# Kernel tuning notes

Hardware: AMD Instinct MI355X
Metric: run time of the kernel (lower is better)

## Reference

```python
import jax, jax.numpy as jnp
import numpy as np

B, S, E, H, L = 8, 1024, 1024, 16, 2
D = E // H
EPS = 1e-5
THRESH = 0.5


def layer_norm(x, g, b):
    mu = x.mean(-1, keepdims=True)
    var = ((x - mu) ** 2).mean(-1, keepdims=True)
    return (x - mu) * jax.lax.rsqrt(var + EPS) * g + b


def mha(x, w_in, w_out):
    # x: [B,S,E]; w_in: [3E,E]; w_out: [E,E] (no biases, PyTorch MultiheadAttention bias=False)
    qkv = x @ w_in.T  # [B,S,3E]
    q, k, v = jnp.split(qkv, 3, axis=-1)
    q = q.reshape(q.shape[0], q.shape[1], H, D).transpose(0, 2, 1, 3)
    k = k.reshape(k.shape[0], k.shape[1], H, D).transpose(0, 2, 1, 3)
    v = v.reshape(v.shape[0], v.shape[1], H, D).transpose(0, 2, 1, 3)
    scores = jnp.einsum('bhqd,bhkd->bhqk', q, k) / jnp.sqrt(jnp.float32(D)).astype(x.dtype)
    attn = jax.nn.softmax(scores, axis=-1)
    out = jnp.einsum('bhqk,bhkd->bhqd', attn, v)
    out = out.transpose(0, 2, 1, 3).reshape(x.shape[0], x.shape[1], E)
    return out @ w_out.T


def thinking_layer(x, w_in, w_out, ffn1, ffn2, g1, b1, g2, b2):
    x = layer_norm(x + mha(x, w_in, w_out), g1, b1)
    h = jax.nn.gelu(x @ ffn1.T, approximate=False) @ ffn2.T
    return layer_norm(x + h, g2, b2)


def setup_inputs() -> dict:
    key = jax.random.key(0)
    ks = jax.random.split(key, 8)
    s = jnp.float32(0.02)
    return {
        'x': jax.random.normal(ks[0], (B, S, E), jnp.float32),
        'w_in': jax.random.normal(ks[1], (L, 3 * E, E), jnp.float32) * s,
        'w_out': jax.random.normal(ks[2], (L, E, E), jnp.float32) * s,
        'ffn_w1': jax.random.normal(ks[3], (L, 4 * E, E), jnp.float32) * s,
        'ffn_w2': jax.random.normal(ks[4], (L, E, 4 * E), jnp.float32) * s,
        'ln1_g': jnp.ones((L, E), jnp.float32),
        'ln1_b': jnp.zeros((L, E), jnp.float32),
        'ln2_g': jnp.ones((L, E), jnp.float32),
        'ln2_b': jnp.zeros((L, E), jnp.float32),
        'ce_w1': jax.random.normal(ks[5], (E // 4, E), jnp.float32) * s,
        'ce_b1': jnp.zeros((E // 4,), jnp.float32),
        'ce_w2': jax.random.normal(ks[6], (1, E // 4), jnp.float32) * s,
        'ce_b2': jnp.zeros((1,), jnp.float32),
        'fast_w': jax.random.normal(ks[7], (E, E), jnp.float32) * s,
    }


def reference(x, w_in, w_out, ffn_w1, ffn_w2, ln1_g, ln1_b, ln2_g, ln2_b,
              ce_w1, ce_b1, ce_w2, ce_b2, fast_w):
    # complexity estimator: mean-pool -> MLP -> logit per batch element
    pooled = x.mean(axis=1)                                   # [B,E]
    h = jax.nn.relu(pooled @ ce_w1.T + ce_b1)                 # [B,E/4]
    logits = (h @ ce_w2.T + ce_b2).squeeze(-1)                # [B]
    probs = jax.nn.sigmoid(logits)
    mode = (probs > THRESH)                                   # eval-mode deterministic routing

    # thinking path (System 2): L stacked attention+FFN layers
    t = x
    for i in range(L):
        t = thinking_layer(t, w_in[i], w_out[i], ffn_w1[i], ffn_w2[i],
                           ln1_g[i], ln1_b[i], ln2_g[i], ln2_b[i])

    # fast path (System 1)
    fast = jax.nn.gelu(x @ fast_w.T, approximate=False)

    out = jnp.where(mode[:, None, None], t, fast)
    mode_f = mode.astype(x.dtype)
    return out, probs, mode_f, mode_f.mean()
```

## Files before the change

### kernel.cpp

```cpp
#include <hip/hip_runtime.h>
#include <cstdint>
#include <cstddef>

#define Bsz 8
#define Ssz 1024
#define Esz 1024
#define Hn  16
#define Dh  64
#define OUT_PROBS 8388608
#define OUT_MODE  8388616
#define OUT_MEAN  8388624

typedef unsigned short u16;
typedef __attribute__((ext_vector_type(8))) __bf16 bf16x8;
typedef __attribute__((ext_vector_type(4))) float  floatx4;

__device__ __forceinline__ float bf2f(u16 u){ return __uint_as_float(((unsigned)u)<<16); }
__device__ __forceinline__ u16 f2bf(float f){
  unsigned u = __float_as_uint(f);
  u += 0x7fffu + ((u>>16)&1u);
  return (u16)(u>>16);
}
__device__ __forceinline__ void unpack2(unsigned u, float& lo, float& hi){
  lo = __uint_as_float(u<<16);
  hi = __uint_as_float(u & 0xffff0000u);
}
__device__ __forceinline__ unsigned pack2(float lo, float hi){
  return (unsigned)f2bf(lo) | ((unsigned)f2bf(hi)<<16);
}
__device__ __forceinline__ void async16(const void* g, void* l){
  __builtin_amdgcn_global_load_lds((const __attribute__((address_space(1))) void*)g,
                                   (__attribute__((address_space(3))) void*)l, 16, 0, 0);
}
__device__ __forceinline__ float gelu_exact(float x){
  return 0.5f*x*(1.0f + erff(x*0.70710678118654752f));
}

struct F2B {
  const float* s[6];
  u16* d[6];
  unsigned end[6];
};

__global__ __launch_bounds__(256)
void f2b_multi(F2B p)
{
  const unsigned i = blockIdx.x*256 + threadIdx.x;
  int k = 0;
  #pragma unroll
  for(int t=0; t<5; t++) if(i >= p.end[t]) k = t+1;
  const unsigned j = i - (k ? p.end[k-1] : 0);
  float4 a = ((const float4*)p.s[k])[2*j];
  float4 b = ((const float4*)p.s[k])[2*j+1];
  uint4 w;
  w.x = pack2(a.x, a.y); w.y = pack2(a.z, a.w);
  w.z = pack2(b.x, b.y); w.w = pack2(b.z, b.w);
  ((uint4*)p.d[k])[j] = w;
}

template<int EPI, int SKIP>
__global__ __launch_bounds__(256, 2)
void gemm_bt(const u16* __restrict__ A, const u16* __restrict__ W,
             void* __restrict__ Cv, const u16* __restrict__ R,
             const float* __restrict__ modes, int N, int K)
{
  const int m0 = blockIdx.x * 128;
  if(SKIP == 1 && modes[m0 >> 10] == 0.0f) return;
  if(SKIP == 2 && modes[m0 >> 10] != 0.0f) return;

  __shared__ __align__(16) u16 AsLo[128*32];
  __shared__ __align__(16) u16 AsHi[128*32];
  __shared__ __align__(16) u16 BsLo[128*32];
  __shared__ __align__(16) u16 BsHi[128*32];

  const int tid  = threadIdx.x;
  const int wave = tid >> 6;
  const int lane = tid & 63;
  const int q    = lane >> 4;
  const int r16  = lane & 15;
  const int wm   = (wave >> 1) * 64;
  const int wn   = (wave & 1) * 64;
  const int n0   = blockIdx.y * 128;

  floatx4 acc[4][4];
  #pragma unroll
  for(int i=0;i<4;i++)
    #pragma unroll
    for(int j=0;j<4;j++){ floatx4 z = {0.f,0.f,0.f,0.f}; acc[i][j] = z; }

  const int row0 = tid >> 2;
  const int kc   = (tid & 3) * 8;

  for(int k0 = 0; k0 < K; k0 += 64){
    __syncthreads();
    async16(A + (size_t)(m0 + row0     )*K + k0 + kc,      AsLo + wave*512);
    async16(A + (size_t)(m0 + row0 + 64)*K + k0 + kc,      AsLo + 2048 + wave*512);
    async16(A + (size_t)(m0 + row0     )*K + k0 + 32 + kc, AsHi + wave*512);
    async16(A + (size_t)(m0 + row0 + 64)*K + k0 + 32 + kc, AsHi + 2048 + wave*512);
    async16(W + (size_t)(n0 + row0     )*K + k0 + kc,      BsLo + wave*512);
    async16(W + (size_t)(n0 + row0 + 64)*K + k0 + kc,      BsLo + 2048 + wave*512);
    async16(W + (size_t)(n0 + row0     )*K + k0 + 32 + kc, BsHi + wave*512);
    async16(W + (size_t)(n0 + row0 + 64)*K + k0 + 32 + kc, BsHi + 2048 + wave*512);
    __syncthreads();

    {
      bf16x8 af[4], bfr[4];
      #pragma unroll
      for(int i=0;i<4;i++){
        af[i]  = *(const bf16x8*)&AsLo[(wm + i*16 + r16)*32 + q*8];
        bfr[i] = *(const bf16x8*)&BsLo[(wn + i*16 + r16)*32 + q*8];
      }
      #pragma unroll
      for(int i=0;i<4;i++)
        #pragma unroll
        for(int j=0;j<4;j++)
          acc[i][j] = __builtin_amdgcn_mfma_f32_16x16x32_bf16(af[i], bfr[j], acc[i][j], 0, 0, 0);
    }
    {
      bf16x8 af[4], bfr[4];
      #pragma unroll
      for(int i=0;i<4;i++){
        af[i]  = *(const bf16x8*)&AsHi[(wm + i*16 + r16)*32 + q*8];
        bfr[i] = *(const bf16x8*)&BsHi[(wn + i*16 + r16)*32 + q*8];
      }
      #pragma unroll
      for(int i=0;i<4;i++)
        #pragma unroll
        for(int j=0;j<4;j++)
          acc[i][j] = __builtin_amdgcn_mfma_f32_16x16x32_bf16(af[i], bfr[j], acc[i][j], 0, 0, 0);
    }
  }

  #pragma unroll
  for(int i=0;i<4;i++){
    const int row = m0 + wm + i*16 + q*4;
    #pragma unroll
    for(int j=0;j<4;j++){
      const int col = n0 + wn + j*16 + r16;
      #pragma unroll
      for(int r=0;r<4;r++){
        float v = acc[i][j][r];
        const size_t idx = (size_t)(row + r)*N + col;
        if(EPI == 1) v += bf2f(R[idx]);
        if(EPI == 2 || EPI == 3) v = gelu_exact(v);
        if(EPI == 3) ((float*)Cv)[idx] = v;
        else         ((u16*)Cv)[idx] = f2bf(v);
      }
    }
  }
}

#define VSTR 68
#define PSTR 72
__global__ __launch_bounds__(256, 4)
void attn_kernel(const u16* __restrict__ qkv, u16* __restrict__ out,
                 const float* __restrict__ modes)
{
  const int bh = blockIdx.x & 127;
  const int b  = bh >> 4;
  if(modes[b] == 0.0f) return;

  __shared__ __align__(16) u16 Qs[2*64*32];
  __shared__ __align__(16) u16 Ks[2*64*32];
  __shared__ __align__(16) u16 Vt[64*VSTR];
  __shared__ __align__(16) u16 Ps[64*PSTR];
  __shared__ float lsump[2][64];

  const int tid = threadIdx.x;
  const int w   = tid >> 6;
  const int lane= tid & 63;
  const int q   = lane >> 4;
  const int r16 = lane & 15;

  const int qt = blockIdx.x >> 7;
  const int h  = bh & 15;
  const int q0 = qt * 64;

  const u16* qbase = qkv + (size_t)(b*Ssz)*3072;

  const int sr = tid >> 2;
  const int sc = (tid & 3) * 8;

  #pragma unroll
  for(int half=0; half<2; half++)
    async16(qbase + (size_t)(q0 + sr)*3072 + h*64 + half*32 + sc,
            &Qs[half*2048 + w*512]);
  __syncthreads();

  const int wm  = (w >> 1) * 32;
  const int wnS = (w & 1) * 32;
  const int wnO = (w & 1) * 32;

  bf16x8 qf[2][2];
  #pragma unroll
  for(int half=0; half<2; half++)
    #pragma unroll
    for(int i=0;i<2;i++)
      qf[half][i] = *(const bf16x8*)&Qs[half*2048 + (wm + i*16 + r16)*32 + q*8];

  floatx4 acc_o[2][2];
  #pragma unroll
  for(int i=0;i<2;i++)
    #pragma unroll
    for(int j=0;j<2;j++){ floatx4 z={0.f,0.f,0.f,0.f}; acc_o[i][j]=z; }
  float ps[2][4] = {{0.f,0.f,0.f,0.f},{0.f,0.f,0.f,0.f}};

  const int kp = tid & 31;
  const int dg = tid >> 5;

  for(int ck=0; ck<16; ck++){
    const int k0 = ck*64;
    __syncthreads();
    #pragma unroll
    for(int half=0; half<2; half++)
      async16(qbase + (size_t)(k0 + sr)*3072 + 1024 + h*64 + half*32 + sc,
              &Ks[half*2048 + w*512]);
    {
      const uint4 va = *(const uint4*)(qbase + (size_t)(k0 + 2*kp    )*3072 + 2048 + h*64 + dg*8);
      const uint4 vb = *(const uint4*)(qbase + (size_t)(k0 + 2*kp + 1)*3072 + 2048 + h*64 + dg*8);
      unsigned wa[4] = {va.x,va.y,va.z,va.w};
      unsigned wb[4] = {vb.x,vb.y,vb.z,vb.w};
      unsigned* vt32 = (unsigned*)Vt;
      #pragma unroll
      for(int u=0; u<4; u++){
        const int d0 = dg*8 + 2*u;
        vt32[(size_t)d0*34 + kp]     = (wa[u] & 0xffffu) | (wb[u] << 16);
        vt32[(size_t)(d0+1)*34 + kp] = (wa[u] >> 16) | (wb[u] & 0xffff0000u);
      }
    }
    __syncthreads();

    floatx4 accS[2][2];
    #pragma unroll
    for(int i=0;i<2;i++)
      #pragma unroll
      for(int j=0;j<2;j++){ floatx4 z={0.f,0.f,0.f,0.f}; accS[i][j]=z; }
    #pragma unroll
    for(int half=0; half<2; half++){
      bf16x8 bf[2];
      #pragma unroll
      for(int j=0;j<2;j++)
        bf[j] = *(const bf16x8*)&Ks[half*2048 + (wnS + j*16 + r16)*32 + q*8];
      #pragma unroll
      for(int i=0;i<2;i++)
        #pragma unroll
        for(int j=0;j<2;j++)
          accS[i][j] = __builtin_amdgcn_mfma_f32_16x16x32_bf16(qf[half][i], bf[j], accS[i][j], 0,0,0);
    }
    #pragma unroll
    for(int i=0;i<2;i++)
      #pragma unroll
      for(int j=0;j<2;j++)
        #pragma unroll
        for(int r=0;r<4;r++){
          const float p = __expf(accS[i][j][r] * 0.125f);
          ps[i][r] += p;
          Ps[(size_t)(wm + i*16 + q*4 + r)*PSTR + wnS + j*16 + r16] = f2bf(p);
        }
    __syncthreads();

    #pragma unroll
    for(int ks=0; ks<2; ks++){
      bf16x8 ap[2], bp[2];
      #pragma unroll
      for(int i=0;i<2;i++)
        ap[i] = *(const bf16x8*)&Ps[(size_t)(wm + i*16 + r16)*PSTR + ks*32 + q*8];
      #pragma unroll
      for(int j=0;j<2;j++)
        bp[j] = *(const bf16x8*)&Vt[(size_t)(wnO + j*16 + r16)*VSTR + ks*32 + q*8];
      #pragma unroll
      for(int i=0;i<2;i++)
        #pragma unroll
        for(int j=0;j<2;j++)
          acc_o[i][j] = __builtin_amdgcn_mfma_f32_16x16x32_bf16(ap[i], bp[j], acc_o[i][j], 0,0,0);
    }
  }

  #pragma unroll
  for(int i=0;i<2;i++)
    #pragma unroll
    for(int r=0;r<4;r++){
      float v = ps[i][r];
      v += __shfl_xor(v, 1, 64);
      v += __shfl_xor(v, 2, 64);
      v += __shfl_xor(v, 4, 64);
      v += __shfl_xor(v, 8, 64);
      ps[i][r] = v;
    }
  if(r16 == 0){
    #pragma unroll
    for(int i=0;i<2;i++)
      #pragma unroll
      for(int r=0;r<4;r++)
        lsump[w & 1][wm + i*16 + q*4 + r] = ps[i][r];
  }
  __syncthreads();

  #pragma unroll
  for(int i=0;i<2;i++)
    #pragma unroll
    for(int r=0;r<4;r++){
      const int row = wm + i*16 + q*4 + r;
      const float inv = 1.0f / (lsump[0][row] + lsump[1][row]);
      #pragma unroll
      for(int j=0;j<2;j++){
        const int col = h*64 + wnO + j*16 + r16;
        out[(size_t)(b*Ssz + q0 + row)*Esz + col] = f2bf(acc_o[i][j][r] * inv);
      }
    }
}

template<int FIN>
__global__ __launch_bounds__(256)
void ln_kernel(const u16* __restrict__ X, const float* __restrict__ G,
               const float* __restrict__ Bi, u16* __restrict__ Y,
               const float* __restrict__ modes, float* __restrict__ outp)
{
  const int row = blockIdx.x;
  if(modes[row >> 10] == 0.0f) return;
  const int tid = threadIdx.x;
  const int wave = tid >> 6, lane = tid & 63;

  uint2 u = ((const uint2*)(X + (size_t)row*Esz))[tid];
  float x0,x1,x2,x3;
  unpack2(u.x, x0, x1); unpack2(u.y, x2, x3);
  float s  = x0+x1+x2+x3;
  float ss = x0*x0 + x1*x1 + x2*x2 + x3*x3;
  #pragma unroll
  for(int off=32; off; off>>=1){
    s  += __shfl_down(s,  off, 64);
    ss += __shfl_down(ss, off, 64);
  }
  __shared__ float rs[4], rss[4], bc[2];
  if(lane == 0){ rs[wave] = s; rss[wave] = ss; }
  __syncthreads();
  if(tid == 0){
    float S  = rs[0]+rs[1]+rs[2]+rs[3];
    float SS = rss[0]+rss[1]+rss[2]+rss[3];
    float mu  = S * (1.0f/1024.0f);
    float var = SS * (1.0f/1024.0f) - mu*mu;
    bc[0] = mu; bc[1] = 1.0f/sqrtf(var + 1e-5f);
  }
  __syncthreads();
  const float mu = bc[0], inv = bc[1];
  float4 g4 = ((const float4*)G)[tid];
  float4 b4 = ((const float4*)Bi)[tid];
  if(FIN){
    float4 o;
    o.x = (x0-mu)*inv*g4.x + b4.x;
    o.y = (x1-mu)*inv*g4.y + b4.y;
    o.z = (x2-mu)*inv*g4.z + b4.z;
    o.w = (x3-mu)*inv*g4.w + b4.w;
    ((float4*)(outp + (size_t)row*Esz))[tid] = o;
  } else {
    uint2 w;
    w.x = pack2((x0-mu)*inv*g4.x + b4.x, (x1-mu)*inv*g4.y + b4.y);
    w.y = pack2((x2-mu)*inv*g4.z + b4.z, (x3-mu)*inv*g4.w + b4.w);
    ((uint2*)(Y + (size_t)row*Esz))[tid] = w;
  }
}

__global__ __launch_bounds__(256)
void pool1_kernel(const float* __restrict__ x, float* __restrict__ part)
{
  const int b = blockIdx.x, tc = blockIdx.y;
  const int e4 = threadIdx.x;
  const float* p = x + (size_t)(b*Ssz + tc*32)*Esz + e4*4;
  float4 s = {0.f,0.f,0.f,0.f};
  for(int t=0; t<32; t++){
    float4 v = *(const float4*)(p + (size_t)t*Esz);
    s.x += v.x; s.y += v.y; s.z += v.z; s.w += v.w;
  }
  ((float4*)(part + (size_t)(b*32 + tc)*Esz))[e4] = s;
}

__global__ void ce1_kernel(const float* __restrict__ part, const float* __restrict__ w1,
                           const float* __restrict__ b1, float* __restrict__ hbuf)
{
  __shared__ float pl[1024];
  const int b = blockIdx.x, n = threadIdx.x;
  for(int i = threadIdx.x; i < 1024; i += 256){
    float s = 0.f;
    for(int tc=0; tc<32; tc++) s += part[(size_t)(b*32 + tc)*Esz + i];
    pl[i] = s * (1.0f/1024.0f);
  }
  __syncthreads();
  const float* wr = w1 + (size_t)n*1024;
  float s = 0.f;
  for(int k=0; k<1024; k++) s += pl[k]*wr[k];
  s += b1[n];
  hbuf[b*256 + n] = fmaxf(s, 0.f);
}

__global__ void ce2_kernel(const float* __restrict__ hbuf, const float* __restrict__ w2,
                           const float* __restrict__ b2, float* __restrict__ modes,
                           float* __restrict__ outp)
{
  const int tid = threadIdx.x;
  const int b = tid >> 5, i = tid & 31;
  float s = 0.f;
  for(int k=i; k<256; k+=32) s += hbuf[b*256 + k] * w2[k];
  #pragma unroll
  for(int off=16; off; off>>=1) s += __shfl_down(s, off, 32);
  __shared__ float md[8];
  if(i == 0){
    const float logit = s + b2[0];
    const float prob = 1.0f/(1.0f + expf(-logit));
    const float m = prob > 0.5f ? 1.0f : 0.0f;
    modes[b] = m; md[b] = m;
    outp[OUT_PROBS + b] = prob;
    outp[OUT_MODE  + b] = m;
  }
  __syncthreads();
  if(tid == 0){
    float acc = 0.f;
    for(int k=0;k<8;k++) acc += md[k];
    outp[OUT_MEAN] = acc * 0.125f;
  }
}

extern "C" void kernel_launch(void* const* d_in, const int* in_sizes, int n_in,
                              void* d_out, int out_size, void* d_ws, size_t ws_size,
                              hipStream_t stream)
{
  const float* x      = (const float*)d_in[0];
  const float* w_in   = (const float*)d_in[1];
  const float* w_out  = (const float*)d_in[2];
  const float* ffn_w1 = (const float*)d_in[3];
  const float* ffn_w2 = (const float*)d_in[4];
  const float* ln1_g  = (const float*)d_in[5];
  const float* ln1_b  = (const float*)d_in[6];
  const float* ln2_g  = (const float*)d_in[7];
  const float* ln2_b  = (const float*)d_in[8];
  const float* ce_w1  = (const float*)d_in[9];
  const float* ce_b1  = (const float*)d_in[10];
  const float* ce_w2  = (const float*)d_in[11];
  const float* ce_b2  = (const float*)d_in[12];
  const float* fast_w = (const float*)d_in[13];
  float* out = (float*)d_out;

  u16* x_bf     = (u16*)d_ws;
  u16* w_in_bf  = x_bf    + (size_t)8192*1024;
  u16* w_out_bf = w_in_bf + (size_t)2*3072*1024;
  u16* ffn1_bf  = w_out_bf+ (size_t)2*1024*1024;
  u16* ffn2_bf  = ffn1_bf + (size_t)2*4096*1024;
  u16* fast_bf  = ffn2_bf + (size_t)2*1024*4096;
  u16* big      = fast_bf + (size_t)1024*1024;
  u16* attn     = big     + (size_t)8192*4096;
  u16* resid    = attn    + (size_t)8192*1024;
  u16* bufA     = resid   + (size_t)8192*1024;
  u16* bufB     = bufA    + (size_t)8192*1024;
  float* part   = (float*)(bufB + (size_t)8192*1024);
  float* hbuf   = part + (size_t)8*32*1024;
  float* modes  = hbuf + 2048;
  const size_t need = (size_t)((char*)(modes + 8) - (char*)d_ws);
  if(ws_size < need) return;

  u16* qkv  = big;
  u16* hmid = big;

  {
    F2B p;
    p.s[0]=x;      p.d[0]=x_bf;     unsigned n0c = 8192u*1024u/8u;
    p.s[1]=w_in;   p.d[1]=w_in_bf;  unsigned n1c = 2u*3072u*1024u/8u;
    p.s[2]=w_out;  p.d[2]=w_out_bf; unsigned n2c = 2u*1024u*1024u/8u;
    p.s[3]=ffn_w1; p.d[3]=ffn1_bf;  unsigned n3c = 2u*4096u*1024u/8u;
    p.s[4]=ffn_w2; p.d[4]=ffn2_bf;  unsigned n4c = 2u*4096u*1024u/8u;
    p.s[5]=fast_w; p.d[5]=fast_bf;  unsigned n5c = 1024u*1024u/8u;
    p.end[0]=n0c; p.end[1]=p.end[0]+n1c; p.end[2]=p.end[1]+n2c;
    p.end[3]=p.end[2]+n3c; p.end[4]=p.end[3]+n4c; p.end[5]=p.end[4]+n5c;
    f2b_multi<<<p.end[5]/256, 256, 0, stream>>>(p);
  }

  pool1_kernel<<<dim3(8,32), 256, 0, stream>>>(x, part);
  ce1_kernel<<<8, 256, 0, stream>>>(part, ce_w1, ce_b1, hbuf);
  ce2_kernel<<<1, 256, 0, stream>>>(hbuf, ce_w2, ce_b2, modes, out);

  const u16* t = x_bf;
  for(int l=0; l<2; l++){
    gemm_bt<0,1><<<dim3(64,24), 256, 0, stream>>>(t, w_in_bf + (size_t)l*3072*1024, qkv, nullptr, modes, 3072, 1024);
    attn_kernel<<<2048, 256, 0, stream>>>(qkv, attn, modes);
    gemm_bt<1,1><<<dim3(64, 8), 256, 0, stream>>>(attn, w_out_bf + (size_t)l*1024*1024, resid, t, modes, 1024, 1024);
    ln_kernel<0><<<8192, 256, 0, stream>>>(resid, ln1_g + l*1024, ln1_b + l*1024, bufA, modes, nullptr);
    gemm_bt<2,1><<<dim3(64,32), 256, 0, stream>>>(bufA, ffn1_bf + (size_t)l*4096*1024, hmid, nullptr, modes, 4096, 1024);
    gemm_bt<1,1><<<dim3(64, 8), 256, 0, stream>>>(hmid, ffn2_bf + (size_t)l*1024*4096, resid, bufA, modes, 1024, 4096);
    if(l == 0)
      ln_kernel<0><<<8192, 256, 0, stream>>>(resid, ln2_g + l*1024, ln2_b + l*1024, bufB, modes, nullptr);
    else
      ln_kernel<1><<<8192, 256, 0, stream>>>(resid, ln2_g + l*1024, ln2_b + l*1024, nullptr, modes, out);
    t = bufB;
  }

  gemm_bt<3,2><<<dim3(64, 8), 256, 0, stream>>>(x_bf, fast_bf, out, nullptr, modes, 1024, 1024);
}
```

Baseline: 913.9 us.

## Use 32x32x16 MFMA tiles in GEMM and tanh-approximate GELU epilogue

```diff
diff --git a/kernel.cpp b/kernel.cpp
--- a/kernel.cpp
+++ b/kernel.cpp
@@ -12,8 +12,9 @@
 #define OUT_MEAN  8388624
 
 typedef unsigned short u16;
-typedef __attribute__((ext_vector_type(8))) __bf16 bf16x8;
-typedef __attribute__((ext_vector_type(4))) float  floatx4;
+typedef __attribute__((ext_vector_type(8)))  __bf16 bf16x8;
+typedef __attribute__((ext_vector_type(4)))  float  floatx4;
+typedef __attribute__((ext_vector_type(16))) float  floatx16;
 
 __device__ __forceinline__ float bf2f(u16 u){ return __uint_as_float(((unsigned)u)<<16); }
 __device__ __forceinline__ u16 f2bf(float f){
@@ -32,8 +33,13 @@
   __builtin_amdgcn_global_load_lds((const __attribute__((address_space(1))) void*)g,
                                    (__attribute__((address_space(3))) void*)l, 16, 0, 0);
 }
-__device__ __forceinline__ float gelu_exact(float x){
-  return 0.5f*x*(1.0f + erff(x*0.70710678118654752f));
+__device__ __forceinline__ float gelu_fast(float x){
+  const float x2 = x*x;
+  const float y  = x * fmaf(0.0356774081f, x2, 0.7978845608f);
+  const float e  = __expf(2.0f*y);
+  const float t  = 1.0f - 2.0f/(e + 1.0f);
+  const float h  = 0.5f*x;
+  return fmaf(h, t, h);
 }
 
 struct F2B {
@@ -76,73 +82,74 @@
   const int tid  = threadIdx.x;
   const int wave = tid >> 6;
   const int lane = tid & 63;
-  const int q    = lane >> 4;
-  const int r16  = lane & 15;
+  const int l31  = lane & 31;
+  const int hw   = lane >> 5;
   const int wm   = (wave >> 1) * 64;
   const int wn   = (wave & 1) * 64;
   const int n0   = blockIdx.y * 128;
 
-  floatx4 acc[4][4];
-  #pragma unroll
-  for(int i=0;i<4;i++)
-    #pragma unroll
-    for(int j=0;j<4;j++){ floatx4 z = {0.f,0.f,0.f,0.f}; acc[i][j] = z; }
+  floatx16 acc[2][2];
+  #pragma unroll
+  for(int i=0;i<2;i++)
+    #pragma unroll
+    for(int j=0;j<2;j++)
+      #pragma unroll
+      for(int r=0;r<16;r++) acc[i][j][r] = 0.f;
 
   const int row0 = tid >> 2;
   const int kc   = (tid & 3) * 8;
 
-  for(int k0 = 0; k0 < K; k0 += 64){
+  const u16* pA0 = A + (size_t)(m0 + row0)*K + kc;
+  const u16* pA1 = pA0 + (size_t)64*K;
+  const u16* pB0 = W + (size_t)(n0 + row0)*K + kc;
+  const u16* pB1 = pB0 + (size_t)64*K;
+
+  for(int k0 = 0; k0 < K; k0 += 64, pA0 += 64, pA1 += 64, pB0 += 64, pB1 += 64){
     __syncthreads();
-    async16(A + (size_t)(m0 + row0     )*K + k0 + kc,      AsLo + wave*512);
-    async16(A + (size_t)(m0 + row0 + 64)*K + k0 + kc,      AsLo + 2048 + wave*512);
-    async16(A + (size_t)(m0 + row0     )*K + k0 + 32 + kc, AsHi + wave*512);
-    async16(A + (size_t)(m0 + row0 + 64)*K + k0 + 32 + kc, AsHi + 2048 + wave*512);
-    async16(W + (size_t)(n0 + row0     )*K + k0 + kc,      BsLo + wave*512);
-    async16(W + (size_t)(n0 + row0 + 64)*K + k0 + kc,      BsLo + 2048 + wave*512);
-    async16(W + (size_t)(n0 + row0     )*K + k0 + 32 + kc, BsHi + wave*512);
-    async16(W + (size_t)(n0 + row0 + 64)*K + k0 + 32 + kc, BsHi + 2048 + wave*512);
+    async16(pA0,      AsLo + wave*512);
+    async16(pA1,      AsLo + 2048 + wave*512);
+    async16(pA0 + 32, AsHi + wave*512);
+    async16(pA1 + 32, AsHi + 2048 + wave*512);
+    async16(pB0,      BsLo + wave*512);
+    async16(pB1,      BsLo + 2048 + wave*512);
+    async16(pB0 + 32, BsHi + wave*512);
+    async16(pB1 + 32, BsHi + 2048 + wave*512);
     __syncthreads();
 
-    {
-      bf16x8 af[4], bfr[4];
-      #pragma unroll
-      for(int i=0;i<4;i++){
-        af[i]  = *(const bf16x8*)&AsLo[(wm + i*16 + r16)*32 + q*8];
-        bfr[i] = *(const bf16x8*)&BsLo[(wn + i*16 + r16)*32 + q*8];
+    #pragma unroll
+    for(int buf=0; buf<2; buf++){
+      const u16* As = buf ? AsHi : AsLo;
+      const u16* Bs = buf ? BsHi : BsLo;
+      #pragma unroll
+      for(int ks=0; ks<2; ks++){
+        const int kb = ks*16 + hw*8;
+        bf16x8 af[2], bfr[2];
+        #pragma unroll
+        for(int i=0;i<2;i++){
+          af[i]  = *(const bf16x8*)&As[(wm + i*32 + l31)*32 + kb];
+          bfr[i] = *(const bf16x8*)&Bs[(wn + i*32 + l31)*32 + kb];
+        }
+        #pragma unroll
+        for(int i=0;i<2;i++)
+          #pragma unroll
+          for(int j=0;j<2;j++)
+            acc[i][j] = __builtin_amdgcn_mfma_f32_32x32x16_bf16(af[i], bfr[j], acc[i][j], 0, 0, 0);
       }
-      #pragma unroll
-      for(int i=0;i<4;i++)
-        #pragma unroll
-        for(int j=0;j<4;j++)
-          acc[i][j] = __builtin_amdgcn_mfma_f32_16x16x32_bf16(af[i], bfr[j], acc[i][j], 0, 0, 0);
-    }
-    {
-      bf16x8 af[4], bfr[4];
-      #pragma unroll
-      for(int i=0;i<4;i++){
-        af[i]  = *(const bf16x8*)&AsHi[(wm + i*16 + r16)*32 + q*8];
-        bfr[i] = *(const bf16x8*)&BsHi[(wn + i*16 + r16)*32 + q*8];
-      }
-      #pragma unroll
-      for(int i=0;i<4;i++)
-        #pragma unroll
-        for(int j=0;j<4;j++)
-          acc[i][j] = __builtin_amdgcn_mfma_f32_16x16x32_bf16(af[i], bfr[j], acc[i][j], 0, 0, 0);
-    }
-  }
-
-  #pragma unroll
-  for(int i=0;i<4;i++){
-    const int row = m0 + wm + i*16 + q*4;
-    #pragma unroll
-    for(int j=0;j<4;j++){
-      const int col = n0 + wn + j*16 + r16;
-      #pragma unroll
-      for(int r=0;r<4;r++){
+    }
+  }
+
+  #pragma unroll
+  for(int i=0;i<2;i++){
+    #pragma unroll
+    for(int j=0;j<2;j++){
+      const int col = n0 + wn + j*32 + l31;
+      #pragma unroll
+      for(int r=0;r<16;r++){
+        const int row = m0 + wm + i*32 + (r&3) + 8*(r>>2) + 4*hw;
         float v = acc[i][j][r];
-        const size_t idx = (size_t)(row + r)*N + col;
+        const size_t idx = (size_t)row*N + col;
         if(EPI == 1) v += bf2f(R[idx]);
-        if(EPI == 2 || EPI == 3) v = gelu_exact(v);
+        if(EPI == 2 || EPI == 3) v = gelu_fast(v);
         if(EPI == 3) ((float*)Cv)[idx] = v;
         else         ((u16*)Cv)[idx] = f2bf(v);
       }
```

New measurement: 986.0 us. +7.9%, slower.
